# Optimization experiments

Measured on AMD Instinct MI355X. Metric: run time of the kernel, lower is better.

Reference implementation:

```python
import jax, jax.numpy as jnp
import numpy as np

B, S = 32, 32
G_RATIO = 0.5
H_W = 1.0
N_STEPS = int(0.95 * S * S)  # training-mode Tmax
SQRT_SIZE = float(np.sqrt(S))
SQRT2 = float(np.sqrt(2.0))

_NF = np.ones((3, 3), np.float32); _NF[1, 1] = 0.0                      # 8-neighbor filter
_CF = np.ones((3, 3), np.float32); _CF[1, 1] = 0.0
_CF[0, 0] = _CF[0, 2] = _CF[2, 0] = _CF[2, 2] = SQRT2                   # diagonal move cost


def conv3x3(x, filt):
    # x: [B,S,S], filt: [3,3] -> SAME conv (matches F.conv2d(padding=1) with one shared filter)
    return jax.lax.conv_general_dilated(x[:, None], filt[None, None], (1, 1), 'SAME')[:, 0]


def diag_heuristic(goal):
    # goal: [B,S,S] one-hot
    ii, jj = jnp.meshgrid(jnp.arange(S), jnp.arange(S), indexing='ij')
    loc = jnp.stack([ii, jj], 0).astype(goal.dtype)                     # [2,S,S]
    goal_loc = jnp.einsum('kij,bij->bk', loc, goal)                     # [B,2]
    dxdy = jnp.abs(loc.reshape(2, -1)[None] - goal_loc[:, :, None])     # [B,2,S*S]
    h = dxdy.min(axis=1) * SQRT2 + jnp.abs(dxdy[:, 0] - dxdy[:, 1])
    return h.reshape(goal.shape)


def astar_core(start, goal, obst):
    nf = jnp.asarray(_NF)
    cf = jnp.asarray(_CF)
    h = diag_heuristic(goal) * H_W
    g0 = jnp.zeros_like(start)
    hist0 = jnp.zeros_like(start)
    goal_idx = jnp.argmax(goal.reshape(B, -1), axis=-1)                 # goal one-hot index
    parents0 = jnp.ones((B, S * S), start.dtype) * goal_idx[:, None].astype(start.dtype)

    def step(carry, _):
        g, open_m, hist, parents, done = carry
        f = G_RATIO * g + (1.0 - G_RATIO + 0.001) * h
        f_exp = jnp.exp(-f / SQRT_SIZE) * open_m
        # straight-through softmax-argmax selection
        v = f_exp.reshape(B, -1)
        y = v / v.sum(-1, keepdims=True)
        ind = jnp.argmax(y, axis=-1)                                    # [B]
        y_hard = jax.nn.one_hot(ind, S * S, dtype=y.dtype)
        sel = (jax.lax.stop_gradient(y_hard - y) + y).reshape(B, S, S)
        dist = (sel * goal).sum((1, 2), keepdims=True)
        unsolved = (dist < 1e-8).astype(f.dtype)
        hist_n = jnp.clip(hist + sel, 0.0, 1.0)
        open_n = jnp.clip(open_m - unsolved * sel, 0.0, 1.0)
        nbr = conv3x3(sel, nf) * obst
        g2 = (g * sel).sum((1, 2), keepdims=True) + conv3x3(sel, cf)
        idx = jax.lax.stop_gradient(
            ((1.0 - open_n) * (1.0 - hist_n) + open_n * (g > g2).astype(f.dtype)) * nbr)
        g_n = jax.lax.stop_gradient(g2 * idx + g * (1.0 - idx))
        open_n = jax.lax.stop_gradient(jnp.clip(open_n + idx, 0.0, 1.0))
        idxf = idx.reshape(B, -1)
        parents_n = ind[:, None].astype(parents.dtype) * idxf + parents * (1.0 - idxf)
        keep = lambda old, new: jnp.where(done, old, new)               # freeze after break point
        carry_n = (keep(g, g_n), keep(open_m, open_n), keep(hist, hist_n),
                   keep(parents, parents_n), done | jnp.all(unsolved == 0))
        return carry_n, None

    init = (g0, start, hist0, parents0, jnp.array(False))
    (g, open_m, hist, parents, done), _ = jax.lax.scan(step, init, None, length=N_STEPS)

    # backtrack (idempotent past the true path length, so run fixed N_STEPS iters)
    pi = jax.lax.stop_gradient(parents).astype(jnp.int32)
    gl = goal.reshape(B, -1).astype(jnp.int32)
    rows = jnp.arange(B)
    loc0 = (pi * gl).sum(-1)

    def bt(i, st):
        path, loc = st
        path = path.at[rows, loc].set(1)
        return path, pi[rows, loc]

    path, _ = jax.lax.fori_loop(0, N_STEPS, bt, (gl, loc0))
    return hist, path.reshape(B, S, S), g


def setup_inputs() -> dict:
    key = jax.random.key(0)
    k1, k2, k3, k4 = jax.random.split(key, 4)
    rows = jnp.arange(B)
    start_idx = jax.random.randint(k2, (B,), 0, S * S // 2)
    goal_idx = jax.random.randint(k3, (B,), S * S // 2, S * S)
    obst = (jax.random.uniform(k1, (B, S, S)) > 0.15).astype(jnp.float32)
    # guarantee start->goal connectivity: clear start's column and goal's row
    obst = obst.at[rows, :, start_idx % S].set(1.0)
    obst = obst.at[rows, goal_idx // S, :].set(1.0)
    start = jax.nn.one_hot(start_idx, S * S, dtype=jnp.float32).reshape(B, 1, S, S)
    goal = jax.nn.one_hot(goal_idx, S * S, dtype=jnp.float32).reshape(B, 1, S, S)
    cost = jax.random.normal(k4, (B, 1, S, S), dtype=jnp.float32)  # unused in 'default' mode
    return {"cost_maps": cost, "start_maps": start, "goal_maps": goal,
            "obstacles_maps": obst[:, None]}


def reference(cost_maps, start_maps, goal_maps, obstacles_maps):
    # mode='default': cost_maps is replaced by zeros in the torch code (unused)
    hist, path, g = astar_core(start_maps[:, 0], goal_maps[:, 0], obstacles_maps[:, 0])
    return hist[:, None], path[:, None], g[:, None]
```

## Files before the change

kernel.cpp:

```cpp
#include <hip/hip_runtime.h>

#define BATCH 32
#define SS 1024
#define NSTEPS 972
#define LSTR 20

#define UNVIS   0x7F000000u
#define CLOSEDB 0x7F000001u
#define OBSTB   0x7F000002u

typedef unsigned long long ull;

template <int CTRL>
__device__ __forceinline__ int dpp32(int v) {
    return __builtin_amdgcn_update_dpp(v, v, CTRL, 0xF, 0xF, false);
}

__device__ __forceinline__ float wave_min_f32_bcast(float v) {
    float t;
    t = __int_as_float(dpp32<0xB1 >(__float_as_int(v))); v = fminf(v, t);
    t = __int_as_float(dpp32<0x4E >(__float_as_int(v))); v = fminf(v, t);
    t = __int_as_float(dpp32<0x141>(__float_as_int(v))); v = fminf(v, t);
    t = __int_as_float(dpp32<0x140>(__float_as_int(v))); v = fminf(v, t);
    t = __int_as_float(dpp32<0x142>(__float_as_int(v))); v = fminf(v, t);
    t = __int_as_float(dpp32<0x143>(__float_as_int(v))); v = fminf(v, t);
    return __int_as_float(__builtin_amdgcn_readlane(__float_as_int(v), 63));
}

__device__ __forceinline__ unsigned umin2(unsigned a, unsigned b) { return a < b ? a : b; }
__device__ __forceinline__ unsigned slotc(float v, unsigned lm, unsigned i) {
    return (__float_as_uint(v) == lm) ? i : 63u;
}

__global__ __launch_bounds__(64)
void astar_kernel(const float* __restrict__ start_maps,
                  const float* __restrict__ goal_maps,
                  const float* __restrict__ obst_maps,
                  float* __restrict__ out)
{
    const int b = blockIdx.x;
    const int lane = threadIdx.x;

    __shared__ __align__(16) float fop[64 * LSTR];
    __shared__ __align__(16) float g_s[SS];
    __shared__ __align__(16) float fh_s[SS];
    __shared__ unsigned short par_s[SS];
    __shared__ int sh_start, sh_goal;

    const float* st = start_maps + b * SS;
    const float* gl = goal_maps + b * SS;
    const float* ob = obst_maps + b * SS;

    for (int i = 0; i < 16; ++i) {
        int c = i * 64 + lane;
        if (st[c] > 0.5f) sh_start = c;
        if (gl[c] > 0.5f) sh_goal = c;
    }
    __syncthreads();
    const int start_idx = sh_start;
    const int goal_idx = sh_goal;
    const float gi = (float)(goal_idx >> 5);
    const float gj = (float)(goal_idx & 31);
    const float SQRT2F = 1.41421356237309515f;
    const float WH = 0.501f;

    for (int i = 0; i < 16; ++i) {
        int c = i * 64 + lane;
        float dx = fabsf((float)(c >> 5) - gi);
        float dy = fabsf((float)(c & 31) - gj);
        float h = __fadd_rn(__fmul_rn(fminf(dx, dy), SQRT2F), fabsf(dx - dy));
        fh_s[c] = __fmul_rn(WH, h);
        g_s[c] = 0.0f;
        par_s[c] = (unsigned short)goal_idx;
        fop[(c >> 4) * LSTR + (c & 15)] = __uint_as_float(ob[c] > 0.5f ? UNVIS : OBSTB);
    }
    __syncthreads();
    if (lane == 0)
        fop[(start_idx >> 4) * LSTR + (start_idx & 15)] = fh_s[start_idx];
    __syncthreads();

    const float* frow = &fop[lane * LSTR];
    float4 r0 = *(const float4*)(frow + 0);
    float4 r1 = *(const float4*)(frow + 4);
    float4 r2 = *(const float4*)(frow + 8);
    float4 r3 = *(const float4*)(frow + 12);
    bool solved = false;

    #pragma unroll 1
    for (int step = 0; step < NSTEPS; ++step) {
        float a0 = fminf(fminf(r0.x, r0.y), fminf(r0.z, r0.w));
        float a1 = fminf(fminf(r1.x, r1.y), fminf(r1.z, r1.w));
        float a2 = fminf(fminf(r2.x, r2.y), fminf(r2.z, r2.w));
        float a3 = fminf(fminf(r3.x, r3.y), fminf(r3.z, r3.w));
        float lmin = fminf(fminf(a0, a1), fminf(a2, a3));
        const unsigned lm = __float_as_uint(lmin);

        unsigned s0 = umin2(umin2(slotc(r0.x, lm, 0),  slotc(r0.y, lm, 1)),
                            umin2(slotc(r0.z, lm, 2),  slotc(r0.w, lm, 3)));
        unsigned s1 = umin2(umin2(slotc(r1.x, lm, 4),  slotc(r1.y, lm, 5)),
                            umin2(slotc(r1.z, lm, 6),  slotc(r1.w, lm, 7)));
        unsigned s2 = umin2(umin2(slotc(r2.x, lm, 8),  slotc(r2.y, lm, 9)),
                            umin2(slotc(r2.z, lm, 10), slotc(r2.w, lm, 11)));
        unsigned s3 = umin2(umin2(slotc(r3.x, lm, 12), slotc(r3.y, lm, 13)),
                            umin2(slotc(r3.z, lm, 14), slotc(r3.w, lm, 15)));
        unsigned slot = umin2(umin2(s0, s1), umin2(s2, s3));

        const float gmin = wave_min_f32_bcast(lmin);
        const ull bal = __ballot(lm == __float_as_uint(gmin));
        const int owner = (int)__builtin_ctzll(bal);
        const int sel = owner * 16 + __builtin_amdgcn_readlane((int)slot, owner);
        solved = (sel == goal_idx);
        const int si = sel >> 5, sj = sel & 31;

        if (lane == 0)
            fop[(sel >> 4) * LSTR + (sel & 15)] = __uint_as_float(CLOSEDB);
        asm volatile("" ::: "memory");

        const float gsel = g_s[sel];

        if (lane < 8) {
            int k = lane < 4 ? lane : lane + 1;
            int di = k / 3 - 1;
            int dj = k - (k / 3) * 3 - 1;
            int ni = si + di, nj = sj + dj;
            if ((unsigned)ni < 32u && (unsigned)nj < 32u) {
                int nb = ni * 32 + nj;
                int fa = (nb >> 4) * LSTR + (nb & 15);
                unsigned fbv = __float_as_uint(fop[fa]);
                float gnb = g_s[nb];
                float fh = fh_s[nb];
                float w = (di != 0 && dj != 0) ? SQRT2F : 1.0f;
                float g2 = __fadd_rn(gsel, w);
                bool rel = (fbv == UNVIS) || (fbv < UNVIS && gnb > g2);
                if (rel) {
                    fop[fa] = __fadd_rn(__fmul_rn(0.5f, g2), fh);
                    g_s[nb] = g2;
                    par_s[nb] = (unsigned short)sel;
                }
            }
        }
        asm volatile("" ::: "memory");
        r0 = *(const float4*)(frow + 0);
        r1 = *(const float4*)(frow + 4);
        r2 = *(const float4*)(frow + 8);
        r3 = *(const float4*)(frow + 12);
        asm volatile("" ::: "memory");

        if (solved) break;
    }

    float* out_hist = out + b * SS;
    float* out_path = out + BATCH * SS + b * SS;
    float* out_g    = out + 2 * BATCH * SS + b * SS;
    for (int i = 0; i < 16; ++i) {
        int c = i * 64 + lane;
        unsigned fbv = __float_as_uint(fop[(c >> 4) * LSTR + (c & 15)]);
        out_hist[c] = (fbv == CLOSEDB) ? 1.0f : 0.0f;
        out_g[c]    = g_s[c];
        out_path[c] = (c == goal_idx) ? 1.0f : 0.0f;
    }
    __syncthreads();
    if (lane == 0) {
        int loc = par_s[goal_idx];
        for (int it = 0; it < NSTEPS; ++it) {
            out_path[loc] = 1.0f;
            if (loc == goal_idx) break;
            loc = par_s[loc];
        }
    }
}

extern "C" void kernel_launch(void* const* d_in, const int* in_sizes, int n_in,
                              void* d_out, int out_size, void* d_ws, size_t ws_size,
                              hipStream_t stream)
{
    const float* start_maps = (const float*)d_in[1];
    const float* goal_maps  = (const float*)d_in[2];
    const float* obst_maps  = (const float*)d_in[3];
    float* out = (float*)d_out;
    hipLaunchKernelGGL(astar_kernel, dim3(BATCH), dim3(64), 0, stream,
                       start_maps, goal_maps, obst_maps, out);
}
```

Baseline: 42.75 us.

## Pipeline A* selection by combining stale-state argmin with fresh relaxed-neighbor keys

Restructures the serial A* loop so each step's global argmin is computed from the previous step's register snapshot, with the selected cell masked out as closed. That result is merged with a small 8-lane reduction over the neighbors freshly relaxed in the previous step. This takes the full wave-wide min and ballot off the critical path after the LDS writes, and uses double-buffered registers so the reload of the next snapshot overlaps the current selection. It adds a 64-bit key packing (f-value bits shifted left by 10, then cell index) and extra register pressure. Correctness depends on the combined key matching the original tie-breaking by lowest index.

```diff
diff --git a/kernel.cpp b/kernel.cpp
--- a/kernel.cpp
+++ b/kernel.cpp
@@ -27,6 +27,21 @@
     return __int_as_float(__builtin_amdgcn_readlane(__float_as_int(v), 63));
 }
 
+template <int CTRL>
+__device__ __forceinline__ ull dpp64(ull k) {
+    unsigned lo = (unsigned)dpp32<CTRL>((int)(unsigned)k);
+    unsigned hi = (unsigned)dpp32<CTRL>((int)(unsigned)(k >> 32));
+    return ((ull)hi << 32) | lo;
+}
+
+__device__ __forceinline__ ull grp8_min_u64(ull k) {
+    ull t;
+    t = dpp64<0xB1 >(k); k = t < k ? t : k;
+    t = dpp64<0x4E >(k); k = t < k ? t : k;
+    t = dpp64<0x141>(k); k = t < k ? t : k;
+    return k;
+}
+
 __device__ __forceinline__ unsigned umin2(unsigned a, unsigned b) { return a < b ? a : b; }
 __device__ __forceinline__ unsigned slotc(float v, unsigned lm, unsigned i) {
     return (__float_as_uint(v) == lm) ? i : 63u;
@@ -80,72 +95,106 @@
     __syncthreads();
 
     const float* frow = &fop[lane * LSTR];
-    float4 r0 = *(const float4*)(frow + 0);
-    float4 r1 = *(const float4*)(frow + 4);
-    float4 r2 = *(const float4*)(frow + 8);
-    float4 r3 = *(const float4*)(frow + 12);
+
+    float4 A0, A1, A2, A3, B0, B1, B2, B3;
+    B0 = *(const float4*)(frow + 0);
+    B1 = *(const float4*)(frow + 4);
+    B2 = *(const float4*)(frow + 8);
+    B3 = *(const float4*)(frow + 12);
+    A0 = B0; A1 = B1; A2 = B2; A3 = B3;
+    ull nk = ~0ull;
+    ull skey = 0;
     bool solved = false;
 
-    #pragma unroll 1
-    for (int step = 0; step < NSTEPS; ++step) {
-        float a0 = fminf(fminf(r0.x, r0.y), fminf(r0.z, r0.w));
-        float a1 = fminf(fminf(r1.x, r1.y), fminf(r1.z, r1.w));
-        float a2 = fminf(fminf(r2.x, r2.y), fminf(r2.z, r2.w));
-        float a3 = fminf(fminf(r3.x, r3.y), fminf(r3.z, r3.w));
+    auto stale_key = [&](float4& q0, float4& q1, float4& q2, float4& q3, int psel) -> ull {
+        const float CB = __uint_as_float(CLOSEDB);
+        int po = psel >> 4, ps = psel & 15;
+        bool own = (lane == po);
+        q0.x = (own && ps == 0 ) ? CB : q0.x;  q0.y = (own && ps == 1 ) ? CB : q0.y;
+        q0.z = (own && ps == 2 ) ? CB : q0.z;  q0.w = (own && ps == 3 ) ? CB : q0.w;
+        q1.x = (own && ps == 4 ) ? CB : q1.x;  q1.y = (own && ps == 5 ) ? CB : q1.y;
+        q1.z = (own && ps == 6 ) ? CB : q1.z;  q1.w = (own && ps == 7 ) ? CB : q1.w;
+        q2.x = (own && ps == 8 ) ? CB : q2.x;  q2.y = (own && ps == 9 ) ? CB : q2.y;
+        q2.z = (own && ps == 10) ? CB : q2.z;  q2.w = (own && ps == 11) ? CB : q2.w;
+        q3.x = (own && ps == 12) ? CB : q3.x;  q3.y = (own && ps == 13) ? CB : q3.y;
+        q3.z = (own && ps == 14) ? CB : q3.z;  q3.w = (own && ps == 15) ? CB : q3.w;
+        float a0 = fminf(fminf(q0.x, q0.y), fminf(q0.z, q0.w));
+        float a1 = fminf(fminf(q1.x, q1.y), fminf(q1.z, q1.w));
+        float a2 = fminf(fminf(q2.x, q2.y), fminf(q2.z, q2.w));
+        float a3 = fminf(fminf(q3.x, q3.y), fminf(q3.z, q3.w));
         float lmin = fminf(fminf(a0, a1), fminf(a2, a3));
-        const unsigned lm = __float_as_uint(lmin);
-
-        unsigned s0 = umin2(umin2(slotc(r0.x, lm, 0),  slotc(r0.y, lm, 1)),
-                            umin2(slotc(r0.z, lm, 2),  slotc(r0.w, lm, 3)));
-        unsigned s1 = umin2(umin2(slotc(r1.x, lm, 4),  slotc(r1.y, lm, 5)),
-                            umin2(slotc(r1.z, lm, 6),  slotc(r1.w, lm, 7)));
-        unsigned s2 = umin2(umin2(slotc(r2.x, lm, 8),  slotc(r2.y, lm, 9)),
-                            umin2(slotc(r2.z, lm, 10), slotc(r2.w, lm, 11)));
-        unsigned s3 = umin2(umin2(slotc(r3.x, lm, 12), slotc(r3.y, lm, 13)),
-                            umin2(slotc(r3.z, lm, 14), slotc(r3.w, lm, 15)));
+        unsigned lm = __float_as_uint(lmin);
+        unsigned s0 = umin2(umin2(slotc(q0.x, lm, 0),  slotc(q0.y, lm, 1)),
+                            umin2(slotc(q0.z, lm, 2),  slotc(q0.w, lm, 3)));
+        unsigned s1 = umin2(umin2(slotc(q1.x, lm, 4),  slotc(q1.y, lm, 5)),
+                            umin2(slotc(q1.z, lm, 6),  slotc(q1.w, lm, 7)));
+        unsigned s2 = umin2(umin2(slotc(q2.x, lm, 8),  slotc(q2.y, lm, 9)),
+                            umin2(slotc(q2.z, lm, 10), slotc(q2.w, lm, 11)));
+        unsigned s3 = umin2(umin2(slotc(q3.x, lm, 12), slotc(q3.y, lm, 13)),
+                            umin2(slotc(q3.z, lm, 14), slotc(q3.w, lm, 15)));
         unsigned slot = umin2(umin2(s0, s1), umin2(s2, s3));
-
-        const float gmin = wave_min_f32_bcast(lmin);
-        const ull bal = __ballot(lm == __float_as_uint(gmin));
-        const int owner = (int)__builtin_ctzll(bal);
-        const int sel = owner * 16 + __builtin_amdgcn_readlane((int)slot, owner);
+        float gmin = wave_min_f32_bcast(lmin);
+        ull bal = __ballot(lm == __float_as_uint(gmin));
+        int owner = (int)__builtin_ctzll(bal);
+        int cell = owner * 16 + __builtin_amdgcn_readlane((int)slot, owner);
+        return (((ull)__float_as_uint(gmin)) << 10) | (unsigned)cell;
+    };
+
+    skey = stale_key(B0, B1, B2, B3, 0x7FFF);
+
+    auto STEP = [&](float4& t0, float4& t1, float4& t2, float4& t3,
+                    float4& l0, float4& l1, float4& l2, float4& l3)
+    {
+        ull red = grp8_min_u64(nk);
+        unsigned frlo = (unsigned)__builtin_amdgcn_readlane((int)(unsigned)red, 0);
+        unsigned frhi = (unsigned)__builtin_amdgcn_readlane((int)(unsigned)(red >> 32), 0);
+        ull fkey = ((ull)frhi << 32) | frlo;
+        ull key = fkey < skey ? fkey : skey;
+        const int sel = (int)(key & 1023ull);
         solved = (sel == goal_idx);
         const int si = sel >> 5, sj = sel & 31;
 
         if (lane == 0)
             fop[(sel >> 4) * LSTR + (sel & 15)] = __uint_as_float(CLOSEDB);
-        asm volatile("" ::: "memory");
-
-        const float gsel = g_s[sel];
-
-        if (lane < 8) {
-            int k = lane < 4 ? lane : lane + 1;
-            int di = k / 3 - 1;
-            int dj = k - (k / 3) * 3 - 1;
-            int ni = si + di, nj = sj + dj;
-            if ((unsigned)ni < 32u && (unsigned)nj < 32u) {
-                int nb = ni * 32 + nj;
-                int fa = (nb >> 4) * LSTR + (nb & 15);
-                unsigned fbv = __float_as_uint(fop[fa]);
-                float gnb = g_s[nb];
-                float fh = fh_s[nb];
-                float w = (di != 0 && dj != 0) ? SQRT2F : 1.0f;
-                float g2 = __fadd_rn(gsel, w);
-                bool rel = (fbv == UNVIS) || (fbv < UNVIS && gnb > g2);
-                if (rel) {
-                    fop[fa] = __fadd_rn(__fmul_rn(0.5f, g2), fh);
-                    g_s[nb] = g2;
-                    par_s[nb] = (unsigned short)sel;
-                }
-            }
+
+        int k8 = lane < 8 ? (lane < 4 ? lane : lane + 1) : 4;
+        int di = k8 / 3 - 1;
+        int dj = k8 - (k8 / 3) * 3 - 1;
+        int ni = si + di, nj = sj + dj;
+        bool act = (lane < 8) && ((unsigned)ni < 32u) && ((unsigned)nj < 32u);
+        int nb = act ? ni * 32 + nj : sel;
+        int fa = (nb >> 4) * LSTR + (nb & 15);
+        unsigned fbv = __float_as_uint(fop[fa]);
+        float gnb = g_s[nb];
+        float fhn = fh_s[nb];
+        float gsel = g_s[sel];
+
+        skey = stale_key(t0, t1, t2, t3, sel);
+
+        nk = ~0ull;
+        float w = ((di != 0) && (dj != 0)) ? SQRT2F : 1.0f;
+        float g2 = __fadd_rn(gsel, w);
+        bool rel = act && ((fbv == UNVIS) || (fbv < UNVIS && gnb > g2));
+        if (rel) {
+            float fnew = __fadd_rn(__fmul_rn(0.5f, g2), fhn);
+            fop[fa] = fnew;
+            g_s[nb] = g2;
+            par_s[nb] = (unsigned short)sel;
+            nk = (((ull)__float_as_uint(fnew)) << 10) | (unsigned)nb;
         }
         asm volatile("" ::: "memory");
-        r0 = *(const float4*)(frow + 0);
-        r1 = *(const float4*)(frow + 4);
-        r2 = *(const float4*)(frow + 8);
-        r3 = *(const float4*)(frow + 12);
+        l0 = *(const float4*)(frow + 0);
+        l1 = *(const float4*)(frow + 4);
+        l2 = *(const float4*)(frow + 8);
+        l3 = *(const float4*)(frow + 12);
         asm volatile("" ::: "memory");
-
+    };
+
+    #pragma unroll 1
+    for (int t = 0; t < NSTEPS; t += 2) {
+        STEP(B0, B1, B2, B3, A0, A1, A2, A3);
+        if (solved) break;
+        STEP(A0, A1, A2, A3, B0, B1, B2, B3);
         if (solved) break;
     }
 
```

Measured after the change: 52.66 us. +23.2%, slower.

## Overlap next-cell argmin with neighbor relaxation using stale row registers

Applied to the files above, without the earlier changes.

Restructures the A* step so the wave-wide argmin over the open set runs on the previous registers, with the just-closed cell masked out. In parallel, the eight neighbor relaxations are evaluated, and their minimum is found with a small 8-lane DPP reduction. The two candidates are then merged with index tie-breaking to pick the next selected cell, which takes the full reduction off the critical path after the LDS stores and reloads. This adds extra per-step arithmetic and relies on the merge being exactly equivalent to a fresh argmin, including tie-breaking order.

```diff
diff --git a/kernel.cpp b/kernel.cpp
--- a/kernel.cpp
+++ b/kernel.cpp
@@ -27,6 +27,14 @@
     return __int_as_float(__builtin_amdgcn_readlane(__float_as_int(v), 63));
 }
 
+__device__ __forceinline__ float grp8_min_f32(float v) {
+    float t;
+    t = __int_as_float(dpp32<0xB1 >(__float_as_int(v))); v = fminf(v, t);
+    t = __int_as_float(dpp32<0x4E >(__float_as_int(v))); v = fminf(v, t);
+    t = __int_as_float(dpp32<0x141>(__float_as_int(v))); v = fminf(v, t);
+    return v;
+}
+
 __device__ __forceinline__ unsigned umin2(unsigned a, unsigned b) { return a < b ? a : b; }
 __device__ __forceinline__ unsigned slotc(float v, unsigned lm, unsigned i) {
     return (__float_as_uint(v) == lm) ? i : 63u;
@@ -80,73 +88,100 @@
     __syncthreads();
 
     const float* frow = &fop[lane * LSTR];
-    float4 r0 = *(const float4*)(frow + 0);
-    float4 r1 = *(const float4*)(frow + 4);
-    float4 r2 = *(const float4*)(frow + 8);
-    float4 r3 = *(const float4*)(frow + 12);
-    bool solved = false;
+    float4 K0 = *(const float4*)(frow + 0);
+    float4 K1 = *(const float4*)(frow + 4);
+    float4 K2 = *(const float4*)(frow + 8);
+    float4 K3 = *(const float4*)(frow + 12);
+
+    const float CB = __uint_as_float(CLOSEDB);
+    const float INFF = __int_as_float(0x7f800000);
+
+    int sel = start_idx;
 
     #pragma unroll 1
     for (int step = 0; step < NSTEPS; ++step) {
-        float a0 = fminf(fminf(r0.x, r0.y), fminf(r0.z, r0.w));
-        float a1 = fminf(fminf(r1.x, r1.y), fminf(r1.z, r1.w));
-        float a2 = fminf(fminf(r2.x, r2.y), fminf(r2.z, r2.w));
-        float a3 = fminf(fminf(r3.x, r3.y), fminf(r3.z, r3.w));
-        float lmin = fminf(fminf(a0, a1), fminf(a2, a3));
-        const unsigned lm = __float_as_uint(lmin);
-
-        unsigned s0 = umin2(umin2(slotc(r0.x, lm, 0),  slotc(r0.y, lm, 1)),
-                            umin2(slotc(r0.z, lm, 2),  slotc(r0.w, lm, 3)));
-        unsigned s1 = umin2(umin2(slotc(r1.x, lm, 4),  slotc(r1.y, lm, 5)),
-                            umin2(slotc(r1.z, lm, 6),  slotc(r1.w, lm, 7)));
-        unsigned s2 = umin2(umin2(slotc(r2.x, lm, 8),  slotc(r2.y, lm, 9)),
-                            umin2(slotc(r2.z, lm, 10), slotc(r2.w, lm, 11)));
-        unsigned s3 = umin2(umin2(slotc(r3.x, lm, 12), slotc(r3.y, lm, 13)),
-                            umin2(slotc(r3.z, lm, 14), slotc(r3.w, lm, 15)));
-        unsigned slot = umin2(umin2(s0, s1), umin2(s2, s3));
-
-        const float gmin = wave_min_f32_bcast(lmin);
-        const ull bal = __ballot(lm == __float_as_uint(gmin));
-        const int owner = (int)__builtin_ctzll(bal);
-        const int sel = owner * 16 + __builtin_amdgcn_readlane((int)slot, owner);
-        solved = (sel == goal_idx);
+        const bool solved = (sel == goal_idx);
         const int si = sel >> 5, sj = sel & 31;
 
         if (lane == 0)
             fop[(sel >> 4) * LSTR + (sel & 15)] = __uint_as_float(CLOSEDB);
         asm volatile("" ::: "memory");
 
-        const float gsel = g_s[sel];
-
-        if (lane < 8) {
-            int k = lane < 4 ? lane : lane + 1;
-            int di = k / 3 - 1;
-            int dj = k - (k / 3) * 3 - 1;
-            int ni = si + di, nj = sj + dj;
-            if ((unsigned)ni < 32u && (unsigned)nj < 32u) {
-                int nb = ni * 32 + nj;
-                int fa = (nb >> 4) * LSTR + (nb & 15);
-                unsigned fbv = __float_as_uint(fop[fa]);
-                float gnb = g_s[nb];
-                float fh = fh_s[nb];
-                float w = (di != 0 && dj != 0) ? SQRT2F : 1.0f;
-                float g2 = __fadd_rn(gsel, w);
-                bool rel = (fbv == UNVIS) || (fbv < UNVIS && gnb > g2);
-                if (rel) {
-                    fop[fa] = __fadd_rn(__fmul_rn(0.5f, g2), fh);
-                    g_s[nb] = g2;
-                    par_s[nb] = (unsigned short)sel;
-                }
-            }
+        int k8 = lane < 8 ? (lane < 4 ? lane : lane + 1) : 4;
+        int di = k8 / 3 - 1;
+        int dj = k8 - (k8 / 3) * 3 - 1;
+        int ni = si + di, nj = sj + dj;
+        bool act = (lane < 8) && ((unsigned)ni < 32u) && ((unsigned)nj < 32u);
+        int nb = act ? ni * 32 + nj : sel;
+        int fa = (nb >> 4) * LSTR + (nb & 15);
+        unsigned fbv = __float_as_uint(fop[fa]);
+        float gnb = g_s[nb];
+        float fhn = fh_s[nb];
+        float gsel = g_s[sel];
+
+        const bool own = (lane == (sel >> 4));
+        const int ps = sel & 15;
+        float q00 = (own && ps == 0 ) ? CB : K0.x;  float q01 = (own && ps == 1 ) ? CB : K0.y;
+        float q02 = (own && ps == 2 ) ? CB : K0.z;  float q03 = (own && ps == 3 ) ? CB : K0.w;
+        float q04 = (own && ps == 4 ) ? CB : K1.x;  float q05 = (own && ps == 5 ) ? CB : K1.y;
+        float q06 = (own && ps == 6 ) ? CB : K1.z;  float q07 = (own && ps == 7 ) ? CB : K1.w;
+        float q08 = (own && ps == 8 ) ? CB : K2.x;  float q09 = (own && ps == 9 ) ? CB : K2.y;
+        float q10 = (own && ps == 10) ? CB : K2.z;  float q11 = (own && ps == 11) ? CB : K2.w;
+        float q12 = (own && ps == 12) ? CB : K3.x;  float q13 = (own && ps == 13) ? CB : K3.y;
+        float q14 = (own && ps == 14) ? CB : K3.z;  float q15 = (own && ps == 15) ? CB : K3.w;
+        float a0 = fminf(fminf(q00, q01), fminf(q02, q03));
+        float a1 = fminf(fminf(q04, q05), fminf(q06, q07));
+        float a2 = fminf(fminf(q08, q09), fminf(q10, q11));
+        float a3 = fminf(fminf(q12, q13), fminf(q14, q15));
+        float lmin = fminf(fminf(a0, a1), fminf(a2, a3));
+        const unsigned lm = __float_as_uint(lmin);
+        unsigned s0 = umin2(umin2(slotc(q00, lm, 0),  slotc(q01, lm, 1)),
+                            umin2(slotc(q02, lm, 2),  slotc(q03, lm, 3)));
+        unsigned s1 = umin2(umin2(slotc(q04, lm, 4),  slotc(q05, lm, 5)),
+                            umin2(slotc(q06, lm, 6),  slotc(q07, lm, 7)));
+        unsigned s2 = umin2(umin2(slotc(q08, lm, 8),  slotc(q09, lm, 9)),
+                            umin2(slotc(q10, lm, 10), slotc(q11, lm, 11)));
+        unsigned s3 = umin2(umin2(slotc(q12, lm, 12), slotc(q13, lm, 13)),
+                            umin2(slotc(q14, lm, 14), slotc(q15, lm, 15)));
+        unsigned slot = umin2(umin2(s0, s1), umin2(s2, s3));
+        const float gmin = wave_min_f32_bcast(lmin);
+        const unsigned sbits = __float_as_uint(gmin);
+        const ull bal = __ballot(lm == sbits);
+        const int owner = (int)__builtin_ctzll(bal);
+        const unsigned scell = (unsigned)(owner * 16 + __builtin_amdgcn_readlane((int)slot, owner));
+
+        float w = ((di != 0) && (dj != 0)) ? SQRT2F : 1.0f;
+        float g2 = __fadd_rn(gsel, w);
+        bool rel = act && ((fbv == UNVIS) || (fbv < UNVIS && gnb > g2));
+        float fnew = __fadd_rn(__fmul_rn(0.5f, g2), fhn);
+        if (rel) fop[fa] = fnew;
+        asm volatile("" ::: "memory");
+
+        K0 = *(const float4*)(frow + 0);
+        K1 = *(const float4*)(frow + 4);
+        K2 = *(const float4*)(frow + 8);
+        K3 = *(const float4*)(frow + 12);
+        asm volatile("" ::: "memory");
+
+        if (rel) {
+            g_s[nb] = g2;
+            par_s[nb] = (unsigned short)sel;
         }
-        asm volatile("" ::: "memory");
-        r0 = *(const float4*)(frow + 0);
-        r1 = *(const float4*)(frow + 4);
-        r2 = *(const float4*)(frow + 8);
-        r3 = *(const float4*)(frow + 12);
-        asm volatile("" ::: "memory");
+
+        float cand = rel ? fnew : INFF;
+        float m8 = grp8_min_f32(cand);
+        const unsigned fbits = (unsigned)__builtin_amdgcn_readlane(__float_as_int(m8), 0);
+        const ull fball = __ballot(rel && (__float_as_uint(cand) == fbits));
+
+        unsigned selnext = scell;
+        if (fball) {
+            int fl = (int)__builtin_ctzll(fball);
+            unsigned fidx = (unsigned)__builtin_amdgcn_readlane(nb, fl);
+            if (fbits < sbits || (fbits == sbits && fidx < scell)) selnext = fidx;
+        }
 
         if (solved) break;
+        sel = (int)selnext;
     }
 
     float* out_hist = out + b * SS;
```

Measured after the change: 52.44 us. +22.6%, slower.

## Overlap frontier reload with neighbor relaxation and compute heuristic on the fly

Applied to the files above, without the earlier changes.

Restructures the step loop so the open-set row reload is issued together with the neighbor reads, before the relaxation stores. Freshly relaxed neighbor f values are folded into the wave-wide min through a second ballot instead of being re-read from LDS after the writes. The heuristic is now computed per neighbor in registers rather than read from a precomputed shared array, which removes that array and its LDS traffic. This shortens the serial LDS dependency chain per step at the cost of an extra ballot and some more ALU work, and tie-breaking between stale and fresh entries must still match the original lowest-index rule.

```diff
diff --git a/kernel.cpp b/kernel.cpp
--- a/kernel.cpp
+++ b/kernel.cpp
@@ -43,7 +43,6 @@
 
     __shared__ __align__(16) float fop[64 * LSTR];
     __shared__ __align__(16) float g_s[SS];
-    __shared__ __align__(16) float fh_s[SS];
     __shared__ unsigned short par_s[SS];
     __shared__ int sh_start, sh_goal;
 
@@ -63,38 +62,76 @@
     const float gj = (float)(goal_idx & 31);
     const float SQRT2F = 1.41421356237309515f;
     const float WH = 0.501f;
+    const float INFF = __int_as_float(0x7f800000);
+    const float CB = __uint_as_float(CLOSEDB);
 
     for (int i = 0; i < 16; ++i) {
         int c = i * 64 + lane;
-        float dx = fabsf((float)(c >> 5) - gi);
-        float dy = fabsf((float)(c & 31) - gj);
-        float h = __fadd_rn(__fmul_rn(fminf(dx, dy), SQRT2F), fabsf(dx - dy));
-        fh_s[c] = __fmul_rn(WH, h);
         g_s[c] = 0.0f;
         par_s[c] = (unsigned short)goal_idx;
         fop[(c >> 4) * LSTR + (c & 15)] = __uint_as_float(ob[c] > 0.5f ? UNVIS : OBSTB);
     }
     __syncthreads();
-    if (lane == 0)
-        fop[(start_idx >> 4) * LSTR + (start_idx & 15)] = fh_s[start_idx];
+    if (lane == 0) {
+        float dx0 = fabsf((float)(start_idx >> 5) - gi);
+        float dy0 = fabsf((float)(start_idx & 31) - gj);
+        float h0 = __fadd_rn(__fmul_rn(fminf(dx0, dy0), SQRT2F), fabsf(dx0 - dy0));
+        fop[(start_idx >> 4) * LSTR + (start_idx & 15)] = __fmul_rn(WH, h0);
+    }
     __syncthreads();
 
     const float* frow = &fop[lane * LSTR];
-    float4 r0 = *(const float4*)(frow + 0);
-    float4 r1 = *(const float4*)(frow + 4);
-    float4 r2 = *(const float4*)(frow + 8);
-    float4 r3 = *(const float4*)(frow + 12);
-    bool solved = false;
+    int sel = start_idx;
 
     #pragma unroll 1
     for (int step = 0; step < NSTEPS; ++step) {
+        const bool solved = (sel == goal_idx);
+        const int si = sel >> 5, sj = sel & 31;
+
+        if (lane == 0)
+            fop[(sel >> 4) * LSTR + (sel & 15)] = CB;
+        asm volatile("" ::: "memory");
+
+        int k8 = lane < 8 ? (lane < 4 ? lane : lane + 1) : 4;
+        int di = k8 / 3 - 1;
+        int dj = k8 - (k8 / 3) * 3 - 1;
+        int ni = si + di, nj = sj + dj;
+        bool act = (lane < 8) && ((unsigned)ni < 32u) && ((unsigned)nj < 32u);
+        int nb = act ? ni * 32 + nj : sel;
+        int fa = (nb >> 4) * LSTR + (nb & 15);
+        unsigned fbv = __float_as_uint(fop[fa]);
+        float gnb = g_s[nb];
+        float gsel = g_s[sel];
+
+        float4 r0 = *(const float4*)(frow + 0);
+        float4 r1 = *(const float4*)(frow + 4);
+        float4 r2 = *(const float4*)(frow + 8);
+        float4 r3 = *(const float4*)(frow + 12);
+        asm volatile("" ::: "memory");
+
+        float dxn = fabsf((float)ni - gi);
+        float dyn = fabsf((float)nj - gj);
+        float hn  = __fadd_rn(__fmul_rn(fminf(dxn, dyn), SQRT2F), fabsf(dxn - dyn));
+        float fhn = __fmul_rn(WH, hn);
+
+        float w = ((di != 0) && (dj != 0)) ? SQRT2F : 1.0f;
+        float g2 = __fadd_rn(gsel, w);
+        bool rel = act && ((fbv == UNVIS) || (fbv < UNVIS && gnb > g2));
+        float fnew = __fadd_rn(__fmul_rn(0.5f, g2), fhn);
+        if (rel) {
+            fop[fa] = fnew;
+            g_s[nb] = g2;
+            par_s[nb] = (unsigned short)sel;
+        }
+        if (solved) break;
+
+        float fv = rel ? fnew : INFF;
         float a0 = fminf(fminf(r0.x, r0.y), fminf(r0.z, r0.w));
         float a1 = fminf(fminf(r1.x, r1.y), fminf(r1.z, r1.w));
         float a2 = fminf(fminf(r2.x, r2.y), fminf(r2.z, r2.w));
         float a3 = fminf(fminf(r3.x, r3.y), fminf(r3.z, r3.w));
         float lmin = fminf(fminf(a0, a1), fminf(a2, a3));
         const unsigned lm = __float_as_uint(lmin);
-
         unsigned s0 = umin2(umin2(slotc(r0.x, lm, 0),  slotc(r0.y, lm, 1)),
                             umin2(slotc(r0.z, lm, 2),  slotc(r0.w, lm, 3)));
         unsigned s1 = umin2(umin2(slotc(r1.x, lm, 4),  slotc(r1.y, lm, 5)),
@@ -105,48 +142,21 @@
                             umin2(slotc(r3.z, lm, 14), slotc(r3.w, lm, 15)));
         unsigned slot = umin2(umin2(s0, s1), umin2(s2, s3));
 
-        const float gmin = wave_min_f32_bcast(lmin);
-        const ull bal = __ballot(lm == __float_as_uint(gmin));
-        const int owner = (int)__builtin_ctzll(bal);
-        const int sel = owner * 16 + __builtin_amdgcn_readlane((int)slot, owner);
-        solved = (sel == goal_idx);
-        const int si = sel >> 5, sj = sel & 31;
+        const float gmin = wave_min_f32_bcast(fminf(lmin, fv));
+        const unsigned gb = __float_as_uint(gmin);
+        const ull bal_s = __ballot(lm == gb);
+        const ull bal_f = __ballot(__float_as_uint(fv) == gb);
 
-        if (lane == 0)
-            fop[(sel >> 4) * LSTR + (sel & 15)] = __uint_as_float(CLOSEDB);
-        asm volatile("" ::: "memory");
-
-        const float gsel = g_s[sel];
-
-        if (lane < 8) {
-            int k = lane < 4 ? lane : lane + 1;
-            int di = k / 3 - 1;
-            int dj = k - (k / 3) * 3 - 1;
-            int ni = si + di, nj = sj + dj;
-            if ((unsigned)ni < 32u && (unsigned)nj < 32u) {
-                int nb = ni * 32 + nj;
-                int fa = (nb >> 4) * LSTR + (nb & 15);
-                unsigned fbv = __float_as_uint(fop[fa]);
-                float gnb = g_s[nb];
-                float fh = fh_s[nb];
-                float w = (di != 0 && dj != 0) ? SQRT2F : 1.0f;
-                float g2 = __fadd_rn(gsel, w);
-                bool rel = (fbv == UNVIS) || (fbv < UNVIS && gnb > g2);
-                if (rel) {
-                    fop[fa] = __fadd_rn(__fmul_rn(0.5f, g2), fh);
-                    g_s[nb] = g2;
-                    par_s[nb] = (unsigned short)sel;
-                }
-            }
+        unsigned idx_s = 0xFFFFu, idx_f = 0xFFFFu;
+        if (bal_s) {
+            int owner = (int)__builtin_ctzll(bal_s);
+            idx_s = (unsigned)(owner * 16 + __builtin_amdgcn_readlane((int)slot, owner));
         }
-        asm volatile("" ::: "memory");
-        r0 = *(const float4*)(frow + 0);
-        r1 = *(const float4*)(frow + 4);
-        r2 = *(const float4*)(frow + 8);
-        r3 = *(const float4*)(frow + 12);
-        asm volatile("" ::: "memory");
-
-        if (solved) break;
+        if (bal_f) {
+            int fl = (int)__builtin_ctzll(bal_f);
+            idx_f = (unsigned)__builtin_amdgcn_readlane(nb, fl);
+        }
+        sel = (int)umin2(idx_s, idx_f);
     }
 
     float* out_hist = out + b * SS;
```

Result: faster. 36.04 us, median of 2 (-15.7%).
